# Kernel tuning notes

Hardware: AMD Instinct MI355X
Metric: run time of the kernel (lower is better)

Reference implementation:

```python
import jax, jax.numpy as jnp
import numpy as np

N, E, D_IN, D_OUT = 100000, 640000, 128, 128


def setup_inputs() -> dict:
    key = jax.random.key(0)
    ks = jax.random.split(key, 8)
    x = jax.random.normal(ks[0], (N, D_IN), dtype=jnp.float32)
    edge_index = jax.random.randint(ks[1], (2, E), 0, N, dtype=jnp.int64)
    s = 1.0 / np.sqrt(D_IN)
    W_lin = jax.random.uniform(ks[2], (D_IN, D_OUT), jnp.float32, -s, s)
    b_lin = jax.random.uniform(ks[3], (D_OUT,), jnp.float32, -s, s)
    W_st = jax.random.uniform(ks[4], (D_IN, D_OUT), jnp.float32, -s, s)
    b_st = jax.random.uniform(ks[5], (D_OUT,), jnp.float32, -s, s)
    W_ts = jax.random.uniform(ks[6], (D_IN, D_OUT), jnp.float32, -s, s)
    b_ts = jax.random.uniform(ks[7], (D_OUT,), jnp.float32, -s, s)
    return {"x": x, "edge_index": edge_index, "W_lin": W_lin, "b_lin": b_lin,
            "W_st": W_st, "b_st": b_st, "W_ts": W_ts, "b_ts": b_ts}


def _scatter_mean(feat_src, idx_dst, num_nodes):
    # gather-then-segment-sum mean aggregation over variable-degree neighborhoods
    summed = jax.ops.segment_sum(feat_src, idx_dst, num_segments=num_nodes)
    cnt = jax.ops.segment_sum(jnp.ones((feat_src.shape[0],), feat_src.dtype),
                              idx_dst, num_segments=num_nodes)
    return summed / jnp.maximum(cnt, 1.0)[:, None]


def reference(x, edge_index, W_lin, b_lin, W_st, b_st, W_ts, b_ts):
    src, dst = edge_index[0], edge_index[1]
    alpha = 0.5
    # SAGEConv(flow='source_to_target', root_weight=False): mean over in-neighbors (src -> dst)
    agg_st = _scatter_mean(x[src], dst, x.shape[0])
    out_st = agg_st @ W_st + b_st
    # SAGEConv(flow='target_to_source'): mean over out-neighbors (dst -> src)
    agg_ts = _scatter_mean(x[dst], src, x.shape[0])
    out_ts = agg_ts @ W_ts + b_ts
    return x @ W_lin + b_lin + (1.0 - alpha) * out_st + alpha * out_ts
```

## Files before the change

kernel.cpp:

```cpp
#include <hip/hip_runtime.h>

#define D    128
#define BROW 32
#define CAPE 31

typedef short short8 __attribute__((ext_vector_type(8)));
typedef float f32x4  __attribute__((ext_vector_type(4)));

static __device__ __forceinline__ unsigned short f2bf(float f) {
    union { float f; unsigned u; } v; v.f = f;
    unsigned r = v.u + 0x7FFFu + ((v.u >> 16) & 1u);
    return (unsigned short)(r >> 16);
}
static __device__ __forceinline__ float bf2f(unsigned short h) {
    union { unsigned u; float f; } v; v.u = ((unsigned)h) << 16;
    return v.f;
}

#define CH 4096

__global__ __launch_bounds__(256) void k_phase0(
    const float* __restrict__ x, const int* __restrict__ ei,
    const float* __restrict__ W_lin, const float* __restrict__ W_st,
    const float* __restrict__ W_ts,
    unsigned short* __restrict__ xb, unsigned short* __restrict__ wtf,
    int* __restrict__ cnt, int* __restrict__ ent,
    int E, int N, int t8, int nbuild, int ncvt)
{
    int b = blockIdx.x;
    if (b < nbuild) {
        const int part  = b & 7;
        const int chunk = b >> 3;
        const int P  = (2 * N + 7) >> 3;
        const int lo = part * P;
        const int hi = lo + P;
        int gg[32], vv[32], pp[32];
        #pragma unroll
        for (int k = 0; k < 16; ++k) {
            int e = chunk * CH + k * 256 + threadIdx.x;
            int s = -1, d = -1;
            if (e < E) { s = ei[e]; d = ei[E + e]; }
            int gts = N + s;
            gg[2 * k]     = (s >= 0 && d >= lo && d < hi) ? d : -1;
            vv[2 * k]     = s;
            gg[2 * k + 1] = (s >= 0 && gts >= lo && gts < hi) ? gts : -1;
            vv[2 * k + 1] = d;
        }
        #pragma unroll
        for (int k = 0; k < 32; ++k)
            if (gg[k] >= 0) pp[k] = atomicAdd(cnt + gg[k], 1);
        __builtin_amdgcn_sched_barrier(0);
        #pragma unroll
        for (int k = 0; k < 32; ++k)
            if (gg[k] >= 0 && pp[k] < CAPE)
                ent[(size_t)gg[k] * BROW + pp[k]] = vv[k];
    } else if (b < nbuild + ncvt) {
        int i = (b - nbuild) * 256 + threadIdx.x;
        if (i >= t8 + D / 8) return;
        if (i >= t8) {
            *((uint4*)(xb + (size_t)i * 8)) = make_uint4(0, 0, 0, 0);
            return;
        }
        const float4* p = (const float4*)(x + (size_t)i * 8);
        float4 a = p[0], c = p[1];
        unsigned r0 = (unsigned)f2bf(a.x) | ((unsigned)f2bf(a.y) << 16);
        unsigned r1 = (unsigned)f2bf(a.z) | ((unsigned)f2bf(a.w) << 16);
        unsigned r2 = (unsigned)f2bf(c.x) | ((unsigned)f2bf(c.y) << 16);
        unsigned r3 = (unsigned)f2bf(c.z) | ((unsigned)f2bf(c.w) << 16);
        *((uint4*)(xb + (size_t)i * 8)) = make_uint4(r0, r1, r2, r3);
    } else {
        int g = (b - nbuild - ncvt) * 256 + threadIdx.x;
        if (g >= 3 * 4 * 8 * 64) return;
        int lane = g & 63;
        int tile = (g >> 6) & 7;
        int ks   = (g >> 9) & 3;
        int m    = g >> 11;
        const float* W = (m == 0) ? W_lin : (m == 1) ? W_st : W_ts;
        float scale = (m == 0) ? 1.0f : 0.5f;
        int n = tile * 16 + (lane & 15);
        int kbase = ks * 32 + (lane >> 4) * 8;
        unsigned short* dst = wtf + (size_t)g * 8;
        #pragma unroll
        for (int j = 0; j < 8; ++j)
            dst[j] = f2bf(W[(size_t)(kbase + j) * D + n] * scale);
    }
}

__global__ __launch_bounds__(256, 7) void k_fused(
    const unsigned short* __restrict__ xb,
    const int* __restrict__ cnt, const int* __restrict__ ent,
    const unsigned short* __restrict__ wtf,
    const float* __restrict__ b_lin, const float* __restrict__ b_st,
    const float* __restrict__ b_ts,
    float* __restrict__ out, int N)
{
    __shared__ unsigned short aggF[2 * 4 * 32 * 4 * 8];

    const int tid  = threadIdx.x;
    const int row0 = blockIdx.x * 32;

    {
        const int grp = tid >> 4;
        const int l16 = tid & 15;
        const unsigned short* xcol = xb + (l16 << 3);

        int slot0 = grp * 4;
        int gn = row0 + (slot0 & 31); if (gn > N - 1) gn = N - 1;
        size_t g = (size_t)(slot0 >> 5) * N + gn;
        const int* row = ent + g * BROW;
        int4 h = *(const int4*)row;
        int dg = cnt[g];

        for (int s = 0; s < 4; ++s) {
            const int* rowN = row; int4 hn = h; int dgn = dg;
            if (s < 3) {
                int slot1 = grp * 4 + s + 1;
                int gn1 = row0 + (slot1 & 31); if (gn1 > N - 1) gn1 = N - 1;
                size_t g1 = (size_t)(slot1 >> 5) * N + gn1;
                rowN = ent + g1 * BROW;
                hn = *(const int4*)rowN;
                dgn = cnt[g1];
            }
            __builtin_amdgcn_sched_barrier(0);
            int slotc = grp * 4 + s;
            int dirc = slotc >> 5, ic = slotc & 31;
            int deg = dg > CAPE ? CAPE : dg;
            int R = (deg + 3) >> 2;

            float a[8];
            #pragma unroll
            for (int t = 0; t < 8; ++t) a[t] = 0.f;

            if (R > 0) {
                int n0 = h.x;
                int n1 = (1 < deg) ? h.y : N;
                int n2 = (2 < deg) ? h.z : N;
                int n3 = (3 < deg) ? h.w : N;
                short8 u0 = *(const short8*)(xcol + (size_t)n0 * D);
                short8 u1 = *(const short8*)(xcol + (size_t)n1 * D);
                short8 u2 = *(const short8*)(xcol + (size_t)n2 * D);
                short8 u3 = *(const short8*)(xcol + (size_t)n3 * D);
                for (int r = 1; r < R; ++r) {
                    int j = r * 4;
                    int m0 = row[j];
                    int m1 = (j + 1 < deg) ? row[j + 1] : N;
                    int m2 = (j + 2 < deg) ? row[j + 2] : N;
                    int m3 = (j + 3 < deg) ? row[j + 3] : N;
                    short8 v0 = *(const short8*)(xcol + (size_t)m0 * D);
                    short8 v1 = *(const short8*)(xcol + (size_t)m1 * D);
                    short8 v2 = *(const short8*)(xcol + (size_t)m2 * D);
                    short8 v3 = *(const short8*)(xcol + (size_t)m3 * D);
                    __builtin_amdgcn_sched_barrier(0);
                    #pragma unroll
                    for (int t = 0; t < 8; ++t)
                        a[t] += (bf2f((unsigned short)u0[t]) + bf2f((unsigned short)u1[t]))
                              + (bf2f((unsigned short)u2[t]) + bf2f((unsigned short)u3[t]));
                    u0 = v0; u1 = v1; u2 = v2; u3 = v3;
                }
                #pragma unroll
                for (int t = 0; t < 8; ++t)
                    a[t] += (bf2f((unsigned short)u0[t]) + bf2f((unsigned short)u1[t]))
                          + (bf2f((unsigned short)u2[t]) + bf2f((unsigned short)u3[t]));
            }

            float inv = 1.0f / fmaxf((float)deg, 1.0f);
            short8 o;
            #pragma unroll
            for (int t = 0; t < 8; ++t) o[t] = (short)f2bf(a[t] * inv);
            ((short8*)aggF)[((dirc * 4 + (l16 >> 2)) * 32 + ic) * 4 + (l16 & 3)] = o;

            row = rowN; h = hn; dg = dgn;
        }
    }

    const int w     = tid >> 6;
    const int lane  = tid & 63;
    const int quad  = lane >> 4;
    const int l15   = lane & 15;
    const int rhalf = w & 1;
    const int tb    = (w >> 1) * 4;
    const int wrow  = rhalf * 16 + l15;
    int rowA = row0 + wrow; if (rowA > N - 1) rowA = N - 1;

    f32x4 acc[4];
    #pragma unroll
    for (int t = 0; t < 4; ++t) acc[t] = (f32x4){0.f, 0.f, 0.f, 0.f};

    {
        short8 a[4];
        const unsigned short* ap = xb + (size_t)rowA * D + quad * 8;
        #pragma unroll
        for (int ks = 0; ks < 4; ++ks)
            a[ks] = *(const short8*)(ap + ks * 32);
        const short8* bw = (const short8*)wtf;
        #pragma unroll
        for (int ks = 0; ks < 4; ++ks) {
            #pragma unroll
            for (int t = 0; t < 4; ++t) {
                short8 bb = bw[(ks * 8 + tb + t) * 64 + lane];
                acc[t] = __builtin_amdgcn_mfma_f32_16x16x32_bf16(a[ks], bb, acc[t], 0, 0, 0);
            }
        }
    }
    __syncthreads();

    for (int m = 1; m < 3; ++m) {
        short8 a[4];
        const short8* af = (const short8*)aggF;
        #pragma unroll
        for (int ks = 0; ks < 4; ++ks)
            a[ks] = af[((m - 1) * 4 + ks) * 128 + wrow * 4 + quad];
        const short8* bw = ((const short8*)wtf) + m * 2048;
        #pragma unroll
        for (int ks = 0; ks < 4; ++ks) {
            #pragma unroll
            for (int t = 0; t < 4; ++t) {
                short8 bb = bw[(ks * 8 + tb + t) * 64 + lane];
                acc[t] = __builtin_amdgcn_mfma_f32_16x16x32_bf16(a[ks], bb, acc[t], 0, 0, 0);
            }
        }
    }

    #pragma unroll
    for (int t = 0; t < 4; ++t) {
        int col = (tb + t) * 16 + l15;
        float bj = b_lin[col] + 0.5f * (b_st[col] + b_ts[col]);
        #pragma unroll
        for (int i = 0; i < 4; ++i) {
            int row = row0 + rhalf * 16 + quad * 4 + i;
            if (row < N)
                __builtin_nontemporal_store(acc[t][i] + bj, &out[(size_t)row * D + col]);
        }
    }
}

extern "C" void kernel_launch(void* const* d_in, const int* in_sizes, int n_in,
                              void* d_out, int out_size, void* d_ws, size_t ws_size,
                              hipStream_t stream)
{
    const float* x     = (const float*)d_in[0];
    const int*   ei    = (const int*)d_in[1];
    const float* W_lin = (const float*)d_in[2];
    const float* b_lin = (const float*)d_in[3];
    const float* W_st  = (const float*)d_in[4];
    const float* b_st  = (const float*)d_in[5];
    const float* W_ts  = (const float*)d_in[6];
    const float* b_ts  = (const float*)d_in[7];
    float*       out   = (float*)d_out;

    const int N = in_sizes[0] / D;
    const int E = in_sizes[1] / 2;
    const int M = 2 * N;

    char* base = (char*)d_ws;
    int* cnt             = (int*)base;            base += (size_t)M * 4;
    int* ent             = (int*)base;            base += (size_t)M * BROW * 4;
    unsigned short* xb   = (unsigned short*)base; base += (size_t)(N + 1) * D * 2;
    unsigned short* wtf  = (unsigned short*)base; base += 3 * 16384 * 2;

    hipMemsetAsync(cnt, 0, (size_t)M * 4, stream);

    const int t8     = N * D / 8;
    const int nbuild = 8 * ((E + CH - 1) / CH);
    const int ncvt   = (t8 + D / 8 + 255) / 256;
    const int nprep  = 24;

    k_phase0<<<dim3(nbuild + ncvt + nprep), dim3(256), 0, stream>>>(
        x, ei, W_lin, W_st, W_ts, xb, wtf, cnt, ent, E, N, t8, nbuild, ncvt);
    k_fused<<<dim3((N + 31) / 32), dim3(256), 0, stream>>>(
        xb, cnt, ent, wtf, b_lin, b_st, b_ts, out, N);
}
```

Before: 244.0 us.

## Gather two 16-byte chunks per lane over 2 slots with cross-slot prefetch

The neighbor-gather phase now assigns 8 lanes per row with 32 bytes each (two short8 loads per neighbor) and handles 2 slots per group instead of 4. The first quad of the second slot is prefetched while the first slot's tail is accumulated. The intent is more bytes in flight per thread and fewer loop iterations, hiding gather latency. The cost is higher register pressure, so launch bounds drop from 7 to 5 waves, which lowers occupancy.

```diff
diff --git a/kernel.cpp b/kernel.cpp
--- a/kernel.cpp
+++ b/kernel.cpp
@@ -86,7 +86,27 @@
     }
 }
 
-__global__ __launch_bounds__(256, 7) void k_fused(
+#define LOADQ(DST, N0, N1, N2, N3) do {                                   \
+    const unsigned short* _p0 = xcol + (size_t)(N0) * D;                  \
+    const unsigned short* _p1 = xcol + (size_t)(N1) * D;                  \
+    const unsigned short* _p2 = xcol + (size_t)(N2) * D;                  \
+    const unsigned short* _p3 = xcol + (size_t)(N3) * D;                  \
+    DST[0] = *(const short8*)_p0; DST[1] = *(const short8*)(_p0 + 8);     \
+    DST[2] = *(const short8*)_p1; DST[3] = *(const short8*)(_p1 + 8);     \
+    DST[4] = *(const short8*)_p2; DST[5] = *(const short8*)(_p2 + 8);     \
+    DST[6] = *(const short8*)_p3; DST[7] = *(const short8*)(_p3 + 8);     \
+} while (0)
+
+#define ACC(A, U) do {                                                    \
+    _Pragma("unroll")                                                     \
+    for (int t = 0; t < 8; ++t) {                                         \
+        A[t]     += (bf2f((unsigned short)U[0][t]) + bf2f((unsigned short)U[2][t]))  \
+                  + (bf2f((unsigned short)U[4][t]) + bf2f((unsigned short)U[6][t])); \
+        A[t + 8] += (bf2f((unsigned short)U[1][t]) + bf2f((unsigned short)U[3][t]))  \
+                  + (bf2f((unsigned short)U[5][t]) + bf2f((unsigned short)U[7][t])); \
+    } } while (0)
+
+__global__ __launch_bounds__(256, 5) void k_fused(
     const unsigned short* __restrict__ xb,
     const int* __restrict__ cnt, const int* __restrict__ ent,
     const unsigned short* __restrict__ wtf,
@@ -100,76 +120,108 @@
     const int row0 = blockIdx.x * 32;
 
     {
-        const int grp = tid >> 4;
-        const int l16 = tid & 15;
-        const unsigned short* xcol = xb + (l16 << 3);
-
-        int slot0 = grp * 4;
-        int gn = row0 + (slot0 & 31); if (gn > N - 1) gn = N - 1;
-        size_t g = (size_t)(slot0 >> 5) * N + gn;
-        const int* row = ent + g * BROW;
-        int4 h = *(const int4*)row;
-        int dg = cnt[g];
-
-        for (int s = 0; s < 4; ++s) {
-            const int* rowN = row; int4 hn = h; int dgn = dg;
-            if (s < 3) {
-                int slot1 = grp * 4 + s + 1;
-                int gn1 = row0 + (slot1 & 31); if (gn1 > N - 1) gn1 = N - 1;
-                size_t g1 = (size_t)(slot1 >> 5) * N + gn1;
-                rowN = ent + g1 * BROW;
-                hn = *(const int4*)rowN;
-                dgn = cnt[g1];
+        const int grp = tid >> 3;
+        const int l8  = tid & 7;
+        const unsigned short* xcol = xb + (l8 << 4);
+
+        const int slot0 = grp * 2, slot1 = slot0 + 1;
+        const int dir0 = slot0 >> 5, is0 = slot0 & 31;
+        const int dir1 = slot1 >> 5, is1 = slot1 & 31;
+        int gn0 = row0 + is0; if (gn0 > N - 1) gn0 = N - 1;
+        int gn1 = row0 + is1; if (gn1 > N - 1) gn1 = N - 1;
+        const size_t g0 = (size_t)dir0 * N + gn0;
+        const size_t g1 = (size_t)dir1 * N + gn1;
+        const int* r0p = ent + g0 * BROW;
+        const int* r1p = ent + g1 * BROW;
+        int4 h0 = *(const int4*)r0p;
+        int4 h1 = *(const int4*)r1p;
+        int dg0 = cnt[g0];
+        int dg1 = cnt[g1];
+        __builtin_amdgcn_sched_barrier(0);
+
+        const int deg0 = dg0 > CAPE ? CAPE : dg0;
+        const int deg1 = dg1 > CAPE ? CAPE : dg1;
+        const int R0 = (deg0 + 3) >> 2;
+        const int R1 = (deg1 + 3) >> 2;
+
+        short8 u[8], v[8];
+        {
+            int n0 = (0 < deg0) ? h0.x : N;
+            int n1 = (1 < deg0) ? h0.y : N;
+            int n2 = (2 < deg0) ? h0.z : N;
+            int n3 = (3 < deg0) ? h0.w : N;
+            LOADQ(u, n0, n1, n2, n3);
+        }
+        float a0[16];
+        #pragma unroll
+        for (int t = 0; t < 16; ++t) a0[t] = 0.f;
+
+        for (int r = 1; r < R0; ++r) {
+            int j = r * 4;
+            int n0 = r0p[j];
+            int n1 = (j + 1 < deg0) ? r0p[j + 1] : N;
+            int n2 = (j + 2 < deg0) ? r0p[j + 2] : N;
+            int n3 = (j + 3 < deg0) ? r0p[j + 3] : N;
+            LOADQ(v, n0, n1, n2, n3);
+            __builtin_amdgcn_sched_barrier(0);
+            ACC(a0, u);
+            #pragma unroll
+            for (int q = 0; q < 8; ++q) u[q] = v[q];
+        }
+        {
+            int n0 = (0 < deg1) ? h1.x : N;
+            int n1 = (1 < deg1) ? h1.y : N;
+            int n2 = (2 < deg1) ? h1.z : N;
+            int n3 = (3 < deg1) ? h1.w : N;
+            LOADQ(v, n0, n1, n2, n3);
+        }
+        __builtin_amdgcn_sched_barrier(0);
+        ACC(a0, u);
+        #pragma unroll
+        for (int q = 0; q < 8; ++q) u[q] = v[q];
+
+        {
+            float inv = 1.0f / fmaxf((float)deg0, 1.0f);
+            short8 olo, ohi;
+            #pragma unroll
+            for (int t = 0; t < 8; ++t) {
+                olo[t] = (short)f2bf(a0[t] * inv);
+                ohi[t] = (short)f2bf(a0[t + 8] * inv);
             }
+            int b0 = ((dir0 * 4 + (l8 >> 1)) * 32 + is0) * 4 + (l8 & 1) * 2;
+            ((short8*)aggF)[b0]     = olo;
+            ((short8*)aggF)[b0 + 1] = ohi;
+        }
+
+        float a1[16];
+        #pragma unroll
+        for (int t = 0; t < 16; ++t) a1[t] = 0.f;
+
+        for (int r = 1; r < R1; ++r) {
+            int j = r * 4;
+            int n0 = r1p[j];
+            int n1 = (j + 1 < deg1) ? r1p[j + 1] : N;
+            int n2 = (j + 2 < deg1) ? r1p[j + 2] : N;
+            int n3 = (j + 3 < deg1) ? r1p[j + 3] : N;
+            LOADQ(v, n0, n1, n2, n3);
             __builtin_amdgcn_sched_barrier(0);
-            int slotc = grp * 4 + s;
-            int dirc = slotc >> 5, ic = slotc & 31;
-            int deg = dg > CAPE ? CAPE : dg;
-            int R = (deg + 3) >> 2;
-
-            float a[8];
-            #pragma unroll
-            for (int t = 0; t < 8; ++t) a[t] = 0.f;
-
-            if (R > 0) {
-                int n0 = h.x;
-                int n1 = (1 < deg) ? h.y : N;
-                int n2 = (2 < deg) ? h.z : N;
-                int n3 = (3 < deg) ? h.w : N;
-                short8 u0 = *(const short8*)(xcol + (size_t)n0 * D);
-                short8 u1 = *(const short8*)(xcol + (size_t)n1 * D);
-                short8 u2 = *(const short8*)(xcol + (size_t)n2 * D);
-                short8 u3 = *(const short8*)(xcol + (size_t)n3 * D);
-                for (int r = 1; r < R; ++r) {
-                    int j = r * 4;
-                    int m0 = row[j];
-                    int m1 = (j + 1 < deg) ? row[j + 1] : N;
-                    int m2 = (j + 2 < deg) ? row[j + 2] : N;
-                    int m3 = (j + 3 < deg) ? row[j + 3] : N;
-                    short8 v0 = *(const short8*)(xcol + (size_t)m0 * D);
-                    short8 v1 = *(const short8*)(xcol + (size_t)m1 * D);
-                    short8 v2 = *(const short8*)(xcol + (size_t)m2 * D);
-                    short8 v3 = *(const short8*)(xcol + (size_t)m3 * D);
-                    __builtin_amdgcn_sched_barrier(0);
-                    #pragma unroll
-                    for (int t = 0; t < 8; ++t)
-                        a[t] += (bf2f((unsigned short)u0[t]) + bf2f((unsigned short)u1[t]))
-                              + (bf2f((unsigned short)u2[t]) + bf2f((unsigned short)u3[t]));
-                    u0 = v0; u1 = v1; u2 = v2; u3 = v3;
-                }
-                #pragma unroll
-                for (int t = 0; t < 8; ++t)
-                    a[t] += (bf2f((unsigned short)u0[t]) + bf2f((unsigned short)u1[t]))
-                          + (bf2f((unsigned short)u2[t]) + bf2f((unsigned short)u3[t]));
+            ACC(a1, u);
+            #pragma unroll
+            for (int q = 0; q < 8; ++q) u[q] = v[q];
+        }
+        ACC(a1, u);
+
+        {
+            float inv = 1.0f / fmaxf((float)deg1, 1.0f);
+            short8 olo, ohi;
+            #pragma unroll
+            for (int t = 0; t < 8; ++t) {
+                olo[t] = (short)f2bf(a1[t] * inv);
+                ohi[t] = (short)f2bf(a1[t + 8] * inv);
             }
-
-            float inv = 1.0f / fmaxf((float)deg, 1.0f);
-            short8 o;
-            #pragma unroll
-            for (int t = 0; t < 8; ++t) o[t] = (short)f2bf(a[t] * inv);
-            ((short8*)aggF)[((dirc * 4 + (l16 >> 2)) * 32 + ic) * 4 + (l16 & 3)] = o;
-
-            row = rowN; h = hn; dg = dgn;
+            int b1 = ((dir1 * 4 + (l8 >> 1)) * 32 + is1) * 4 + (l8 & 1) * 2;
+            ((short8*)aggF)[b1]     = olo;
+            ((short8*)aggF)[b1 + 1] = ohi;
         }
     }
 
```

Measured after the change: 253.3 us. 1.04x slower.
